# Performance work log

Hardware: AMD Instinct MI355X
Metric: run time of the kernel (lower is better)

## Reference

```python
import jax, jax.numpy as jnp
import numpy as np
from jax import lax

WINDOW_SIZE = 11
SIGMA = 1.5
DATA_RANGE = 1.0
K1, K2 = 0.01, 0.03


def _gaussian_window(window_size, sigma):
    coords = jnp.arange(window_size, dtype=jnp.float32) - window_size // 2
    g = jnp.exp(-coords ** 2 / (2.0 * sigma ** 2))
    g = g / g.sum()
    w = g[:, None] * g[None, :]                      # (k,k)
    return w[None, None, :, :]                       # (1,1,k,k) OIHW


def setup_inputs() -> dict:
    key = jax.random.key(0)
    k1, k2 = jax.random.split(key)
    shape = (16, 3, 512, 512)
    img1 = jax.random.uniform(k1, shape, dtype=jnp.float32)
    img2 = jax.random.uniform(k2, shape, dtype=jnp.float32)
    return {"img1": img1, "img2": img2}


def _ssim_loss(img1, img2):
    B, C, H, W = img1.shape
    pad = WINDOW_SIZE // 2
    window = _gaussian_window(WINDOW_SIZE, SIGMA).astype(img1.dtype)
    C1 = (K1 * DATA_RANGE) ** 2
    C2 = (K2 * DATA_RANGE) ** 2

    x1 = img1.reshape(B * C, 1, H, W)
    x2 = img2.reshape(B * C, 1, H, W)
    # Stack the five quantities along the batch axis -> single conv call.
    stacked = jnp.concatenate([x1, x2, x1 * x1, x2 * x2, x1 * x2], axis=0)
    stacked = jnp.pad(stacked, ((0, 0), (0, 0), (pad, pad), (pad, pad)), mode="reflect")
    blurred = lax.conv_general_dilated(
        stacked, window, window_strides=(1, 1), padding="VALID",
        dimension_numbers=("NCHW", "OIHW", "NCHW"))
    mu1, mu2, e11, e22, e12 = [
        b.reshape(B, C, H, W) for b in jnp.split(blurred, 5, axis=0)
    ]

    mu1_sq = mu1 * mu1
    mu2_sq = mu2 * mu2
    mu1_mu2 = mu1 * mu2
    sigma1_sq = e11 - mu1_sq
    sigma2_sq = e22 - mu2_sq
    sigma12 = e12 - mu1_mu2

    ssim_map = ((2.0 * mu1_mu2 + C1) * (2.0 * sigma12 + C2)) / (
        (mu1_sq + mu2_sq + C1) * (sigma1_sq + sigma2_sq + C2))
    ssim_map = jnp.clip(ssim_map, 0.0, 1.0)
    return 1.0 - jnp.mean(ssim_map)


def reference(img1, img2):
    return _ssim_loss(img1, img2)
```

## Files before the change

### kernel.cpp

```cpp
#include <hip/hip_runtime.h>
#include <hip/hip_fp16.h>

#define NIMG   48
#define H      512
#define W      512
#define CH     16
#define RCH    32
#define CCH    4
#define CW     128
#define NTHR   64
#define LDSW   144
#define HT     26
#define NBLOCK (NIMG * RCH * CCH)
#define NPIX   12582912.0f

__device__ __forceinline__ int refl(int x) {
    x = (x < 0) ? -x : x;
    return (x >= 512) ? (1022 - x) : x;
}

static constexpr float GWc[11] = {
    0.00102838f, 0.00759876f, 0.03600075f, 0.10936075f, 0.21300700f,
    0.26601190f, 0.21300700f, 0.10936075f, 0.03600075f, 0.00759876f,
    0.00102838f};

__device__ __forceinline__ float ssim_from(__half2 M, __half2 E,
                                           float C1, float C2) {
    const float mup = __low2float(M);
    const float mud = __high2float(M);
    const float esp = __low2float(E);
    const float ed  = __high2float(E);
    const float mus = mup + 1.0f;
    const float P   = mus * mus;
    const float Q   = mud * mud;
    const float Vs  = esp - mup * mup;
    const float Vd  = ed  - mud * mud;
    const float num = fmaf(0.5f, P - Q,  C1) * fmaf(0.5f, Vs - Vd, C2);
    const float den = fmaf(0.5f, P + Q,  C1) * fmaf(0.5f, Vs + Vd, C2);
    float s = num * __builtin_amdgcn_rcpf(den);
    return fminf(fmaxf(s, 0.f), 1.f);
}

__global__ __launch_bounds__(NTHR, 6)
void ssim_main(const float* __restrict__ img1, const float* __restrict__ img2,
               float* __restrict__ partial) {
    __shared__ __half2 sdl[11][LDSW];

    const int t     = threadIdx.x;
    const int xb    = blockIdx.x & 3;
    const int chunk = (blockIdx.x >> 2) & (RCH - 1);
    const int img   = blockIdx.x >> 7;
    const int C0    = xb * CW;
    const int R0    = chunk * CH;

    const float* __restrict__ b1 = img1 + (size_t)img * (H * W);
    const float* __restrict__ b2 = img2 + (size_t)img * (H * W);

    const int gc0 = refl(C0 - 5 + t);
    const int gc1 = refl(C0 - 5 + t + 64);
    const int gc2 = (t + 128 < 138) ? refl(C0 - 5 + t + 128) : 0;
    const bool l2 = (t + 128) < 138;

    __half2 wh[11];
#pragma unroll
    for (int k = 0; k < 11; ++k) wh[k] = __float2half2_rn(GWc[k]);

    __half2 pA[11], pB[11], pC[11], pD[11];
#pragma unroll
    for (int i = 0; i < 11; ++i) {
        pA[i] = __float2half2_rn(0.f); pB[i] = pA[i];
        pC[i] = pA[i];                 pD[i] = pA[i];
    }

    float acc = 0.f;
    const float C1 = 0.0001f, C2 = 0.0009f;

    for (int grp = 0; grp < 3; ++grp) {
        const int base  = grp * 11;
        const int nrows = (grp == 2) ? (HT - 22) : 11;
        __syncthreads();
        for (int p = 0; p < nrows; ++p) {
            const int jr = refl(R0 - 5 + base + p);
            const float* r1 = b1 + jr * W;
            const float* r2 = b2 + jr * W;
            {
                const float a0 = r1[gc0], b0 = r2[gc0];
                const float a1 = r1[gc1], b1v = r2[gc1];
                sdl[p][t]      = __floats2half2_rn(a0 + b0 - 1.0f, a0 - b0);
                sdl[p][t + 64] = __floats2half2_rn(a1 + b1v - 1.0f, a1 - b1v);
                if (l2) {
                    const float a2 = r1[gc2], b2v = r2[gc2];
                    sdl[p][t + 128] = __floats2half2_rn(a2 + b2v - 1.0f, a2 - b2v);
                }
            }
        }
        __syncthreads();

#pragma unroll
        for (int p = 0; p < 11; ++p) {
            const int jj = base + p;
            if (jj < HT) {
                const float2* wp = (const float2*)(&sdl[p][2 * t]);
                float2 wr[6];
#pragma unroll
                for (int r = 0; r < 6; ++r) wr[r] = wp[r];
                __half2 sd[12];
#pragma unroll
                for (int r = 0; r < 6; ++r) {
                    sd[2 * r]     = __builtin_bit_cast(__half2, wr[r].x);
                    sd[2 * r + 1] = __builtin_bit_cast(__half2, wr[r].y);
                }
                __half2 sq[12];
#pragma unroll
                for (int j = 0; j < 12; ++j) sq[j] = __hmul2(sd[j], sd[j]);

                __half2 hM0 = __float2half2_rn(0.f), hE0 = hM0;
                __half2 hM1 = hM0, hE1 = hM0;
#pragma unroll
                for (int k = 0; k < 11; ++k) {
                    hM0 = __hfma2(wh[k], sd[k],     hM0);
                    hE0 = __hfma2(wh[k], sq[k],     hE0);
                    hM1 = __hfma2(wh[k], sd[k + 1], hM1);
                    hE1 = __hfma2(wh[k], sq[k + 1], hE1);
                }

#pragma unroll
                for (int s_ = 0; s_ < 11; ++s_) {
                    const int dd = (p - s_ + 11) % 11;
                    if (dd == 0) {
                        pA[s_] = __hmul2(wh[0], hM0);
                        pB[s_] = __hmul2(wh[0], hM1);
                        pC[s_] = __hmul2(wh[0], hE0);
                        pD[s_] = __hmul2(wh[0], hE1);
                    } else if (dd == 10) {
                        if (jj >= 10) {
                            const __half2 A  = __hfma2(wh[10], hM0, pA[s_]);
                            const __half2 B  = __hfma2(wh[10], hM1, pB[s_]);
                            const __half2 Cq = __hfma2(wh[10], hE0, pC[s_]);
                            const __half2 Dq = __hfma2(wh[10], hE1, pD[s_]);
                            acc += ssim_from(A, Cq, C1, C2);
                            acc += ssim_from(B, Dq, C1, C2);
                        }
                    } else {
                        pA[s_] = __hfma2(wh[dd], hM0, pA[s_]);
                        pB[s_] = __hfma2(wh[dd], hM1, pB[s_]);
                        pC[s_] = __hfma2(wh[dd], hE0, pC[s_]);
                        pD[s_] = __hfma2(wh[dd], hE1, pD[s_]);
                    }
                }
            }
        }
    }

#pragma unroll
    for (int off = 32; off > 0; off >>= 1) acc += __shfl_xor(acc, off);
    if (t == 0) partial[blockIdx.x] = acc;
}

__global__ void ssim_finish(const float* __restrict__ partial, float* __restrict__ out) {
    float s = 0.f;
    for (int i = threadIdx.x; i < NBLOCK; i += 256) s += partial[i];
#pragma unroll
    for (int off = 32; off > 0; off >>= 1) s += __shfl_xor(s, off);
    __shared__ float wred[4];
    if ((threadIdx.x & 63) == 0) wred[threadIdx.x >> 6] = s;
    __syncthreads();
    if (threadIdx.x == 0)
        out[0] = 1.0f - (wred[0] + wred[1] + wred[2] + wred[3]) / NPIX;
}

extern "C" void kernel_launch(void* const* d_in, const int* in_sizes, int n_in,
                              void* d_out, int out_size, void* d_ws, size_t ws_size,
                              hipStream_t stream) {
    const float* img1 = (const float*)d_in[0];
    const float* img2 = (const float*)d_in[1];
    float* out = (float*)d_out;
    float* partial = (float*)d_ws;
    ssim_main<<<NBLOCK, NTHR, 0, stream>>>(img1, img2, partial);
    ssim_finish<<<1, 256, 0, stream>>>(partial, out);
}
```

Measured before the change: 160.7 us.

## Stream rows through double-buffered LDS with register prefetch of next row

Replaces the three-phase load-11-rows-then-compute scheme with a per-row software pipeline: the next row's global loads are issued into registers before the current row's LDS-backed convolution runs, then written into a two-row LDS ping-pong buffer. The loop is fully unrolled so ring-buffer indices are compile-time, and the vertical accumulation skips outputs outside the chunk. The intent is to hide global load latency behind compute and cut LDS footprint. In exchange it adds a barrier per row and lowers the launch-bounds occupancy hint from 6 to 4, which raises register pressure headroom but may reduce waves per CU.

```diff
diff --git a/kernel.cpp b/kernel.cpp
--- a/kernel.cpp
+++ b/kernel.cpp
@@ -41,10 +41,10 @@
     return fminf(fmaxf(s, 0.f), 1.f);
 }
 
-__global__ __launch_bounds__(NTHR, 6)
+__global__ __launch_bounds__(NTHR, 4)
 void ssim_main(const float* __restrict__ img1, const float* __restrict__ img2,
                float* __restrict__ partial) {
-    __shared__ __half2 sdl[11][LDSW];
+    __shared__ __half2 Cb[2][LDSW];
 
     const int t     = threadIdx.x;
     const int xb    = blockIdx.x & 3;
@@ -58,98 +58,100 @@
 
     const int gc0 = refl(C0 - 5 + t);
     const int gc1 = refl(C0 - 5 + t + 64);
-    const int gc2 = (t + 128 < 138) ? refl(C0 - 5 + t + 128) : 0;
-    const bool l2 = (t + 128) < 138;
+    const bool l2 = t < 10;
+    const int gc2 = l2 ? refl(C0 - 5 + t + 128) : 0;
 
     __half2 wh[11];
 #pragma unroll
     for (int k = 0; k < 11; ++k) wh[k] = __float2half2_rn(GWc[k]);
 
     __half2 pA[11], pB[11], pC[11], pD[11];
-#pragma unroll
-    for (int i = 0; i < 11; ++i) {
-        pA[i] = __float2half2_rn(0.f); pB[i] = pA[i];
-        pC[i] = pA[i];                 pD[i] = pA[i];
-    }
 
     float acc = 0.f;
     const float C1 = 0.0001f, C2 = 0.0009f;
 
-    for (int grp = 0; grp < 3; ++grp) {
-        const int base  = grp * 11;
-        const int nrows = (grp == 2) ? (HT - 22) : 11;
-        __syncthreads();
-        for (int p = 0; p < nrows; ++p) {
-            const int jr = refl(R0 - 5 + base + p);
+    {
+        const int jr = refl(R0 - 5);
+        const float* r1 = b1 + jr * W;
+        const float* r2 = b2 + jr * W;
+        const float a0 = r1[gc0], b0 = r2[gc0];
+        const float a1 = r1[gc1], b1v = r2[gc1];
+        Cb[0][t]      = __floats2half2_rn(a0 + b0 - 1.0f, a0 - b0);
+        Cb[0][t + 64] = __floats2half2_rn(a1 + b1v - 1.0f, a1 - b1v);
+        if (l2) {
+            const float a2 = r1[gc2], b2v = r2[gc2];
+            Cb[0][t + 128] = __floats2half2_rn(a2 + b2v - 1.0f, a2 - b2v);
+        }
+    }
+    __syncthreads();
+
+#pragma unroll
+    for (int jj = 0; jj < HT; ++jj) {
+        const int cur = jj & 1, nxt = cur ^ 1;
+
+        float a0 = 0.f, b0 = 0.f, a1 = 0.f, b1v = 0.f, a2 = 0.f, b2v = 0.f;
+        if (jj + 1 < HT) {
+            const int jr = refl(R0 - 5 + jj + 1);
             const float* r1 = b1 + jr * W;
             const float* r2 = b2 + jr * W;
-            {
-                const float a0 = r1[gc0], b0 = r2[gc0];
-                const float a1 = r1[gc1], b1v = r2[gc1];
-                sdl[p][t]      = __floats2half2_rn(a0 + b0 - 1.0f, a0 - b0);
-                sdl[p][t + 64] = __floats2half2_rn(a1 + b1v - 1.0f, a1 - b1v);
-                if (l2) {
-                    const float a2 = r1[gc2], b2v = r2[gc2];
-                    sdl[p][t + 128] = __floats2half2_rn(a2 + b2v - 1.0f, a2 - b2v);
-                }
+            a0 = r1[gc0]; b0 = r2[gc0];
+            a1 = r1[gc1]; b1v = r2[gc1];
+            if (l2) { a2 = r1[gc2]; b2v = r2[gc2]; }
+        }
+
+        const float2* wp = (const float2*)(&Cb[cur][2 * t]);
+        float2 wr[6];
+#pragma unroll
+        for (int r = 0; r < 6; ++r) wr[r] = wp[r];
+        __half2 sd[12];
+#pragma unroll
+        for (int r = 0; r < 6; ++r) {
+            sd[2 * r]     = __builtin_bit_cast(__half2, wr[r].x);
+            sd[2 * r + 1] = __builtin_bit_cast(__half2, wr[r].y);
+        }
+        __half2 sq[12];
+#pragma unroll
+        for (int j = 0; j < 12; ++j) sq[j] = __hmul2(sd[j], sd[j]);
+
+        __half2 hM0 = __float2half2_rn(0.f), hE0 = hM0;
+        __half2 hM1 = hM0, hE1 = hM0;
+#pragma unroll
+        for (int k = 0; k < 11; ++k) {
+            hM0 = __hfma2(wh[k], sd[k],     hM0);
+            hE0 = __hfma2(wh[k], sq[k],     hE0);
+            hM1 = __hfma2(wh[k], sd[k + 1], hM1);
+            hE1 = __hfma2(wh[k], sq[k + 1], hE1);
+        }
+
+#pragma unroll
+        for (int dd = 0; dd <= 10; ++dd) {
+            const int rr = jj - dd;
+            if (rr < 0 || rr >= CH) continue;
+            const int s = rr % 11;
+            if (dd == 0) {
+                pA[s] = __hmul2(wh[0], hM0);
+                pB[s] = __hmul2(wh[0], hM1);
+                pC[s] = __hmul2(wh[0], hE0);
+                pD[s] = __hmul2(wh[0], hE1);
+            } else {
+                pA[s] = __hfma2(wh[dd], hM0, pA[s]);
+                pB[s] = __hfma2(wh[dd], hM1, pB[s]);
+                pC[s] = __hfma2(wh[dd], hE0, pC[s]);
+                pD[s] = __hfma2(wh[dd], hE1, pD[s]);
+            }
+            if (dd == 10) {
+                acc += ssim_from(pA[s], pC[s], C1, C2);
+                acc += ssim_from(pB[s], pD[s], C1, C2);
             }
         }
+
+        if (jj + 1 < HT) {
+            Cb[nxt][t]      = __floats2half2_rn(a0 + b0 - 1.0f, a0 - b0);
+            Cb[nxt][t + 64] = __floats2half2_rn(a1 + b1v - 1.0f, a1 - b1v);
+            if (l2)
+                Cb[nxt][t + 128] = __floats2half2_rn(a2 + b2v - 1.0f, a2 - b2v);
+        }
         __syncthreads();
-
-#pragma unroll
-        for (int p = 0; p < 11; ++p) {
-            const int jj = base + p;
-            if (jj < HT) {
-                const float2* wp = (const float2*)(&sdl[p][2 * t]);
-                float2 wr[6];
-#pragma unroll
-                for (int r = 0; r < 6; ++r) wr[r] = wp[r];
-                __half2 sd[12];
-#pragma unroll
-                for (int r = 0; r < 6; ++r) {
-                    sd[2 * r]     = __builtin_bit_cast(__half2, wr[r].x);
-                    sd[2 * r + 1] = __builtin_bit_cast(__half2, wr[r].y);
-                }
-                __half2 sq[12];
-#pragma unroll
-                for (int j = 0; j < 12; ++j) sq[j] = __hmul2(sd[j], sd[j]);
-
-                __half2 hM0 = __float2half2_rn(0.f), hE0 = hM0;
-                __half2 hM1 = hM0, hE1 = hM0;
-#pragma unroll
-                for (int k = 0; k < 11; ++k) {
-                    hM0 = __hfma2(wh[k], sd[k],     hM0);
-                    hE0 = __hfma2(wh[k], sq[k],     hE0);
-                    hM1 = __hfma2(wh[k], sd[k + 1], hM1);
-                    hE1 = __hfma2(wh[k], sq[k + 1], hE1);
-                }
-
-#pragma unroll
-                for (int s_ = 0; s_ < 11; ++s_) {
-                    const int dd = (p - s_ + 11) % 11;
-                    if (dd == 0) {
-                        pA[s_] = __hmul2(wh[0], hM0);
-                        pB[s_] = __hmul2(wh[0], hM1);
-                        pC[s_] = __hmul2(wh[0], hE0);
-                        pD[s_] = __hmul2(wh[0], hE1);
-                    } else if (dd == 10) {
-                        if (jj >= 10) {
-                            const __half2 A  = __hfma2(wh[10], hM0, pA[s_]);
-                            const __half2 B  = __hfma2(wh[10], hM1, pB[s_]);
-                            const __half2 Cq = __hfma2(wh[10], hE0, pC[s_]);
-                            const __half2 Dq = __hfma2(wh[10], hE1, pD[s_]);
-                            acc += ssim_from(A, Cq, C1, C2);
-                            acc += ssim_from(B, Dq, C1, C2);
-                        }
-                    } else {
-                        pA[s_] = __hfma2(wh[dd], hM0, pA[s_]);
-                        pB[s_] = __hfma2(wh[dd], hM1, pB[s_]);
-                        pC[s_] = __hfma2(wh[dd], hE0, pC[s_]);
-                        pD[s_] = __hfma2(wh[dd], hE1, pD[s_]);
-                    }
-                }
-            }
-        }
     }
 
 #pragma unroll
```

Result: slower. 257.4 us (+60.2%).

## Double-buffer LDS row staging to overlap global loads with convolution compute

Applied to the files above, without the earlier changes.

Rows for the next 11-row group are loaded from global memory into registers before each row's compute and written into a second LDS buffer afterwards. This removes the serialized load phase and one barrier per group, hiding global latency behind the FMA work. The cost is doubled LDS usage, extra live registers, and a lowered launch-bounds occupancy hint (6 to 5 blocks).

```diff
diff --git a/kernel.cpp b/kernel.cpp
--- a/kernel.cpp
+++ b/kernel.cpp
@@ -41,10 +41,10 @@
     return fminf(fmaxf(s, 0.f), 1.f);
 }
 
-__global__ __launch_bounds__(NTHR, 6)
+__global__ __launch_bounds__(NTHR, 5)
 void ssim_main(const float* __restrict__ img1, const float* __restrict__ img2,
                float* __restrict__ partial) {
-    __shared__ __half2 sdl[11][LDSW];
+    __shared__ __half2 sdl[2][11][LDSW];
 
     const int t     = threadIdx.x;
     const int xb    = blockIdx.x & 3;
@@ -58,8 +58,8 @@
 
     const int gc0 = refl(C0 - 5 + t);
     const int gc1 = refl(C0 - 5 + t + 64);
-    const int gc2 = (t + 128 < 138) ? refl(C0 - 5 + t + 128) : 0;
-    const bool l2 = (t + 128) < 138;
+    const bool l2 = t < 10;
+    const int gc2 = l2 ? refl(C0 - 5 + t + 128) : 0;
 
     __half2 wh[11];
 #pragma unroll
@@ -75,32 +75,42 @@
     float acc = 0.f;
     const float C1 = 0.0001f, C2 = 0.0009f;
 
+    for (int p = 0; p < 11; ++p) {
+        const int jr = refl(R0 - 5 + p);
+        const float* r1 = b1 + jr * W;
+        const float* r2 = b2 + jr * W;
+        const float a0 = r1[gc0], b0 = r2[gc0];
+        const float a1 = r1[gc1], b1v = r2[gc1];
+        sdl[0][p][t]      = __floats2half2_rn(a0 + b0 - 1.0f, a0 - b0);
+        sdl[0][p][t + 64] = __floats2half2_rn(a1 + b1v - 1.0f, a1 - b1v);
+        if (l2) {
+            const float a2 = r1[gc2], b2v = r2[gc2];
+            sdl[0][p][t + 128] = __floats2half2_rn(a2 + b2v - 1.0f, a2 - b2v);
+        }
+    }
+
     for (int grp = 0; grp < 3; ++grp) {
-        const int base  = grp * 11;
-        const int nrows = (grp == 2) ? (HT - 22) : 11;
+        const int base = grp * 11;
+        const int cur  = grp & 1, nxt = cur ^ 1;
         __syncthreads();
-        for (int p = 0; p < nrows; ++p) {
-            const int jr = refl(R0 - 5 + base + p);
-            const float* r1 = b1 + jr * W;
-            const float* r2 = b2 + jr * W;
-            {
-                const float a0 = r1[gc0], b0 = r2[gc0];
-                const float a1 = r1[gc1], b1v = r2[gc1];
-                sdl[p][t]      = __floats2half2_rn(a0 + b0 - 1.0f, a0 - b0);
-                sdl[p][t + 64] = __floats2half2_rn(a1 + b1v - 1.0f, a1 - b1v);
-                if (l2) {
-                    const float a2 = r1[gc2], b2v = r2[gc2];
-                    sdl[p][t + 128] = __floats2half2_rn(a2 + b2v - 1.0f, a2 - b2v);
-                }
-            }
-        }
-        __syncthreads();
-
 #pragma unroll
         for (int p = 0; p < 11; ++p) {
             const int jj = base + p;
+            const int jn = jj + 11;
+            const bool doStage = (jn < HT);
+
+            float a0 = 0.f, b0 = 0.f, a1 = 0.f, b1v = 0.f, a2 = 0.f, b2v = 0.f;
+            if (doStage) {
+                const int jr = refl(R0 - 5 + jn);
+                const float* r1 = b1 + jr * W;
+                const float* r2 = b2 + jr * W;
+                a0 = r1[gc0]; b0 = r2[gc0];
+                a1 = r1[gc1]; b1v = r2[gc1];
+                if (l2) { a2 = r1[gc2]; b2v = r2[gc2]; }
+            }
+
             if (jj < HT) {
-                const float2* wp = (const float2*)(&sdl[p][2 * t]);
+                const float2* wp = (const float2*)(&sdl[cur][p][2 * t]);
                 float2 wr[6];
 #pragma unroll
                 for (int r = 0; r < 6; ++r) wr[r] = wp[r];
@@ -149,6 +159,13 @@
                     }
                 }
             }
+
+            if (doStage) {
+                sdl[nxt][p][t]      = __floats2half2_rn(a0 + b0 - 1.0f, a0 - b0);
+                sdl[nxt][p][t + 64] = __floats2half2_rn(a1 + b1v - 1.0f, a1 - b1v);
+                if (l2)
+                    sdl[nxt][p][t + 128] = __floats2half2_rn(a2 + b2v - 1.0f, a2 - b2v);
+            }
         }
     }
 
```

Result: slower. 170.2 us (+5.9%).
